# Kernel optimization log

Hardware: AMD Instinct MI355X
Metric: run time of the kernel (lower is better)

## Reference

```python
import jax, jax.numpy as jnp
import numpy as np

NUM_HEADS = 4
HEAD_DIM = 64
RHO = 0.1  # threshold_rho


def setup_inputs() -> dict:
    key = jax.random.key(0)
    k0, k1, k2, k3, k4 = jax.random.split(key, 5)
    B, L, D = 2, 225, 256  # grid_size=15 -> L=225
    Hd = NUM_HEADS * HEAD_DIM
    w_scale = 1.0 / np.sqrt(D)
    return {
        "x": jax.random.normal(k0, (B, L, D), dtype=jnp.float32),
        "Wq": jax.random.normal(k1, (Hd, D), dtype=jnp.float32) * w_scale,
        "Wk": jax.random.normal(k2, (Hd, D), dtype=jnp.float32) * w_scale,
        "Wv": jax.random.normal(k3, (Hd, D), dtype=jnp.float32) * w_scale,
        "Wo": jax.random.normal(k4, (D, Hd), dtype=jnp.float32) * w_scale,
    }


def reference(x, Wq, Wk, Wv, Wo):
    B, L, D = x.shape
    H, d = NUM_HEADS, HEAD_DIM
    # Projections (torch Linear: y = x @ W.T), split heads -> [B,H,L,d]
    q = (x @ Wq.T).reshape(B, L, H, d).transpose(0, 2, 1, 3)
    k = (x @ Wk.T).reshape(B, L, H, d).transpose(0, 2, 1, 3)
    v = (x @ Wv.T).reshape(B, L, H, d).transpose(0, 2, 1, 3)

    # Raw attention scores S = Q K^T  [B,H,L,L]
    S = jnp.einsum('bhid,bhjd->bhij', q, k)

    # Adjacency build: for each key column j, U_j = s_j s_j^T / d, zero diag,
    # keep entries > rho; A = mean over j. Vectorized over j: [B,H,Li,Lk,Lj].
    eye = jnp.eye(L, dtype=S.dtype)
    U = S[:, :, :, None, :] * S[:, :, None, :, :] / d      # [B,H,i,k,j]
    U = U * (1.0 - eye)[None, None, :, :, None]            # zero (i==k) diag
    A = jnp.where(U > RHO, U, 0.0).sum(axis=-1) / L        # [B,H,L,L]

    # Normalize: A_hat = D^-1/2 (A + I) D^-1/2
    A_tilde = A + eye
    deg = jnp.clip(A_tilde.sum(axis=-1, keepdims=True), 1e-6, None)
    d_inv_sqrt = deg ** -0.5
    A_hat = d_inv_sqrt * A_tilde * jnp.swapaxes(d_inv_sqrt, -1, -2)

    # Jump: Phi(S) = A_hat S A_hat^T, then scale and softmax-attend
    S_jump = jnp.einsum('bhij,bhjk,bhlk->bhil', A_hat, S, A_hat) / np.sqrt(d)
    attn = jax.nn.softmax(S_jump, axis=-1)
    out = jnp.einsum('bhij,bhjd->bhid', attn, v)           # [B,H,L,d]
    out = out.transpose(0, 2, 1, 3).reshape(B, L, H * d)
    return out @ Wo.T
```

## Files before the change

### kernel.cpp

```cpp
#include <hip/hip_runtime.h>
#include <math.h>

#define B_  2
#define L_  225
#define D_  256
#define H_  4
#define DH_ 64
#define BH_ (B_*H_)
#define M_  (B_*L_)
#define LL_ (L_*L_)
#define RHO 0.1f
#define INV_L (1.0f/225.0f)
#define INV_SQRT_D 0.125f

__device__ __forceinline__ float dinv_of(const float* deg, int idx) {
    return 1.0f / sqrtf(fmaxf(deg[idx], 1e-6f));
}

__global__ __launch_bounds__(256) void k_qkv(
    const float* __restrict__ x, const float* __restrict__ Wq,
    const float* __restrict__ Wk, const float* __restrict__ Wv,
    float* __restrict__ q, float* __restrict__ k, float* __restrict__ v,
    float* __restrict__ deg)
{
    const int t = threadIdx.x;
    if (blockIdx.z == 0 && blockIdx.y == 0 && t < 128) {
        int idx = blockIdx.x * 128 + t;
        if (idx < BH_ * L_) deg[idx] = 1.0f;
    }
    const int which = blockIdx.z;
    const float* W = (which == 0) ? Wq : (which == 1) ? Wk : Wv;
    float* out = (which == 0) ? q : (which == 1) ? k : v;
    const int m0 = blockIdx.x * 32;
    const int n0 = blockIdx.y * 32;
    __shared__ float Xs[32][36];
    __shared__ float Ws[32][36];
    const int ty = t >> 4, tx = t & 15;
    const int sr = t >> 3, sc4 = (t & 7) * 4;
    float acc[2][2] = {};
    for (int kt = 0; kt < D_; kt += 32) {
        int m = m0 + sr;
        float4 xv = (m < M_) ? *(const float4*)&x[m * D_ + kt + sc4]
                             : make_float4(0.f, 0.f, 0.f, 0.f);
        float4 wv = *(const float4*)&W[(n0 + sr) * D_ + kt + sc4];
        *(float4*)&Xs[sr][sc4] = xv;
        *(float4*)&Ws[sr][sc4] = wv;
        __syncthreads();
        #pragma unroll
        for (int kk = 0; kk < 32; ++kk) {
            float a0 = Xs[ty*2+0][kk], a1 = Xs[ty*2+1][kk];
            float b0 = Ws[tx*2+0][kk], b1 = Ws[tx*2+1][kk];
            acc[0][0] += a0*b0; acc[0][1] += a0*b1;
            acc[1][0] += a1*b0; acc[1][1] += a1*b1;
        }
        __syncthreads();
    }
    #pragma unroll
    for (int i = 0; i < 2; ++i) {
        int m = m0 + ty*2 + i;
        if (m >= M_) continue;
        int b = m / L_, l = m % L_;
        #pragma unroll
        for (int j = 0; j < 2; ++j) {
            int n = n0 + tx*2 + j;
            int h = n >> 6, dd = n & 63;
            out[((b * H_ + h) * L_ + l) * DH_ + dd] = acc[i][j];
        }
    }
}

__global__ __launch_bounds__(256) void k_scores(
    const float* __restrict__ q, const float* __restrict__ kk_,
    float* __restrict__ S)
{
    const int bh = blockIdx.z;
    const int i0 = blockIdx.x * 32, j0 = blockIdx.y * 32;
    __shared__ float Qs[32][68], Ks[32][68];
    const float* qb = q + bh * L_ * DH_;
    const float* kb = kk_ + bh * L_ * DH_;
    const int t = threadIdx.x;
    #pragma unroll
    for (int s = 0; s < 2; ++s) {
        int li = t + s * 256;
        int r = li >> 4, c4 = (li & 15) * 4;
        float4 qv = (i0 + r < L_) ? *(const float4*)&qb[(i0 + r) * DH_ + c4]
                                  : make_float4(0.f,0.f,0.f,0.f);
        float4 kv = (j0 + r < L_) ? *(const float4*)&kb[(j0 + r) * DH_ + c4]
                                  : make_float4(0.f,0.f,0.f,0.f);
        *(float4*)&Qs[r][c4] = qv;
        *(float4*)&Ks[r][c4] = kv;
    }
    __syncthreads();
    const int ty = t >> 4, tx = t & 15;
    float acc[2][2] = {};
    #pragma unroll
    for (int c = 0; c < 64; ++c) {
        float a0 = Qs[ty*2+0][c], a1 = Qs[ty*2+1][c];
        float b0 = Ks[tx*2+0][c], b1 = Ks[tx*2+1][c];
        acc[0][0] += a0*b0; acc[0][1] += a0*b1;
        acc[1][0] += a1*b0; acc[1][1] += a1*b1;
    }
    float* Sb = S + bh * LL_;
    #pragma unroll
    for (int i = 0; i < 2; ++i) {
        int gi = i0 + ty*2 + i;
        if (gi >= L_) continue;
        #pragma unroll
        for (int j = 0; j < 2; ++j) {
            int gj = j0 + tx*2 + j;
            if (gj < L_) Sb[gi * L_ + gj] = acc[i][j];
        }
    }
}

__global__ __launch_bounds__(256) void k_adj(
    const float* __restrict__ S, float* __restrict__ A, float* __restrict__ deg)
{
    const int bh = blockIdx.z;
    const int i0 = blockIdx.x * 32, k0 = blockIdx.y * 32;
    __shared__ float SiT[32][34], SkT[32][34];
    const float* Sb = S + bh * LL_;
    const int t = threadIdx.x;
    const int tx = t & 15, ty = t >> 4;
    float a00 = 0.f, a01 = 0.f, a10 = 0.f, a11 = 0.f;
    for (int jc = 0; jc < L_; jc += 32) {
        #pragma unroll
        for (int s = 0; s < 4; ++s) {
            int li = t + s * 256;
            int r = li >> 5, c = li & 31;
            int j = jc + c;
            SiT[c][r] = (i0 + r < L_ && j < L_) ? Sb[(i0 + r) * L_ + j] * 0.125f : 0.f;
            SkT[c][r] = (k0 + r < L_ && j < L_) ? Sb[(k0 + r) * L_ + j] * 0.125f : 0.f;
        }
        __syncthreads();
        #pragma unroll
        for (int j = 0; j < 32; ++j) {
            float2 a = *(const float2*)&SiT[j][ty * 2];
            float2 b = *(const float2*)&SkT[j][tx * 2];
            float u;
            u = a.x * b.x; a00 += (u > RHO) ? u : 0.f;
            u = a.x * b.y; a01 += (u > RHO) ? u : 0.f;
            u = a.y * b.x; a10 += (u > RHO) ? u : 0.f;
            u = a.y * b.y; a11 += (u > RHO) ? u : 0.f;
        }
        __syncthreads();
    }
    const int gi0 = i0 + ty * 2, gk0 = k0 + tx * 2;
    float v00 = (gi0     < L_ && gk0     < L_ && gi0     != gk0    ) ? a00 * INV_L : 0.f;
    float v01 = (gi0     < L_ && gk0 + 1 < L_ && gi0     != gk0 + 1) ? a01 * INV_L : 0.f;
    float v10 = (gi0 + 1 < L_ && gk0     < L_ && gi0 + 1 != gk0    ) ? a10 * INV_L : 0.f;
    float v11 = (gi0 + 1 < L_ && gk0 + 1 < L_ && gi0 + 1 != gk0 + 1) ? a11 * INV_L : 0.f;
    float* Ab = A + bh * LL_;
    if (gi0 < L_) {
        if (gk0     < L_) Ab[gi0 * L_ + gk0    ] = v00;
        if (gk0 + 1 < L_) Ab[gi0 * L_ + gk0 + 1] = v01;
    }
    if (gi0 + 1 < L_) {
        if (gk0     < L_) Ab[(gi0+1) * L_ + gk0    ] = v10;
        if (gk0 + 1 < L_) Ab[(gi0+1) * L_ + gk0 + 1] = v11;
    }
    float rs0 = v00 + v01, rs1 = v10 + v11;
    #pragma unroll
    for (int m = 1; m < 16; m <<= 1) {
        rs0 += __shfl_xor(rs0, m);
        rs1 += __shfl_xor(rs1, m);
    }
    if (tx == 0) {
        if (gi0     < L_) atomicAdd(&deg[bh * L_ + gi0    ], rs0);
        if (gi0 + 1 < L_) atomicAdd(&deg[bh * L_ + gi0 + 1], rs1);
    }
}

__global__ __launch_bounds__(256) void k_m1(
    const float* __restrict__ A, const float* __restrict__ S,
    const float* __restrict__ deg, float* __restrict__ M1)
{
    const int bh = blockIdx.z;
    const int i0 = blockIdx.x * 32, c0 = blockIdx.y * 32;
    __shared__ float As[32][33];
    __shared__ float Ss[32][34];
    const float* Ab = A + bh * LL_;
    const float* Sb = S + bh * LL_;
    const float* db = deg + bh * L_;
    const int t = threadIdx.x;
    const int ty = t >> 4, tx = t & 15;
    float acc[2][2] = {};
    for (int jt = 0; jt < L_; jt += 32) {
        #pragma unroll
        for (int s = 0; s < 4; ++s) {
            int li = t + s * 256;
            int r = li >> 5, c = li & 31;
            int gi = i0 + r, gj = jt + c;
            float av = (gi < L_ && gj < L_) ? Ab[gi * L_ + gj] : 0.f;
            if (gi == gj && gi < L_) av += 1.f;
            As[r][c] = av;
            int gj2 = jt + r, gc = c0 + c;
            float sv = 0.f;
            if (gj2 < L_ && gc < L_) sv = Sb[gj2 * L_ + gc] * dinv_of(db, gj2);
            Ss[r][c] = sv;
        }
        __syncthreads();
        #pragma unroll
        for (int kk = 0; kk < 32; ++kk) {
            float a0 = As[ty*2+0][kk], a1 = As[ty*2+1][kk];
            float2 b = *(const float2*)&Ss[kk][tx * 2];
            acc[0][0] += a0*b.x; acc[0][1] += a0*b.y;
            acc[1][0] += a1*b.x; acc[1][1] += a1*b.y;
        }
        __syncthreads();
    }
    float* Mb = M1 + bh * LL_;
    #pragma unroll
    for (int i = 0; i < 2; ++i) {
        int gi = i0 + ty*2 + i;
        if (gi >= L_) continue;
        float dvi = dinv_of(db, gi);
        #pragma unroll
        for (int j = 0; j < 2; ++j) {
            int gc = c0 + tx*2 + j;
            if (gc < L_) Mb[gi * L_ + gc] = acc[i][j] * dvi;
        }
    }
}

__global__ __launch_bounds__(256) void k_sjump(
    const float* __restrict__ M1, const float* __restrict__ A,
    const float* __restrict__ deg, float* __restrict__ attn)
{
    const int bh = blockIdx.z;
    const int i0 = blockIdx.x * 32, l0 = blockIdx.y * 32;
    __shared__ float Ms[32][33];
    __shared__ float Bs[32][33];
    const float* Mb = M1 + bh * LL_;
    const float* Ab = A + bh * LL_;
    const float* db = deg + bh * L_;
    const int t = threadIdx.x;
    const int ty = t >> 4, tx = t & 15;
    float acc[2][2] = {};
    for (int jt = 0; jt < L_; jt += 32) {
        #pragma unroll
        for (int s = 0; s < 4; ++s) {
            int li = t + s * 256;
            int r = li >> 5, c = li & 31;
            int gi = i0 + r, gj = jt + c;
            Ms[r][c] = (gi < L_ && gj < L_) ? Mb[gi * L_ + gj] : 0.f;
            int gl = l0 + r;
            float bv = 0.f;
            if (gl < L_ && gj < L_) {
                bv = Ab[gl * L_ + gj];
                if (gl == gj) bv += 1.f;
                bv *= dinv_of(db, gj);
            }
            Bs[r][c] = bv;
        }
        __syncthreads();
        #pragma unroll
        for (int kk = 0; kk < 32; ++kk) {
            float a0 = Ms[ty*2+0][kk], a1 = Ms[ty*2+1][kk];
            float b0 = Bs[tx*2+0][kk], b1 = Bs[tx*2+1][kk];
            acc[0][0] += a0*b0; acc[0][1] += a0*b1;
            acc[1][0] += a1*b0; acc[1][1] += a1*b1;
        }
        __syncthreads();
    }
    float* ob = attn + bh * LL_;
    #pragma unroll
    for (int i = 0; i < 2; ++i) {
        int gi = i0 + ty*2 + i;
        if (gi >= L_) continue;
        #pragma unroll
        for (int j = 0; j < 2; ++j) {
            int gl = l0 + tx*2 + j;
            if (gl < L_) ob[gi * L_ + gl] = acc[i][j] * dinv_of(db, gl) * INV_SQRT_D;
        }
    }
}

__global__ __launch_bounds__(256) void k_smav(
    const float* __restrict__ sj, const float* __restrict__ v,
    float* __restrict__ oh)
{
    const int bh = blockIdx.y, i0 = blockIdx.x * 16;
    __shared__ float P[16][226];
    __shared__ float rinv[16];
    const float* sb = sj + bh * LL_;
    const float* vb = v + bh * L_ * DH_;
    const int t = threadIdx.x;
    for (int e = t; e < 16 * L_; e += 256) {
        int r = e / L_, c = e - r * L_;
        int gi = i0 + r;
        P[r][c] = (gi < L_) ? sb[gi * L_ + c] : 0.f;
    }
    __syncthreads();
    {
        const int r = t >> 4, lane = t & 15;
        float m = -INFINITY;
        for (int c = lane; c < L_; c += 16) m = fmaxf(m, P[r][c]);
        #pragma unroll
        for (int mk = 1; mk < 16; mk <<= 1) m = fmaxf(m, __shfl_xor(m, mk));
        float ssum = 0.f;
        for (int c = lane; c < L_; c += 16) {
            float e = expf(P[r][c] - m);
            P[r][c] = e;
            ssum += e;
        }
        #pragma unroll
        for (int mk = 1; mk < 16; mk <<= 1) ssum += __shfl_xor(ssum, mk);
        if (lane == 0) rinv[r] = 1.0f / ssum;
    }
    __syncthreads();
    const int dd = t & 63, rg = t >> 6;
    float acc[4] = {};
    for (int l = 0; l < L_; ++l) {
        float vv = vb[l * DH_ + dd];
        #pragma unroll
        for (int u = 0; u < 4; ++u) acc[u] += P[rg * 4 + u][l] * vv;
    }
    const int b = bh >> 2, h = bh & 3;
    #pragma unroll
    for (int u = 0; u < 4; ++u) {
        int r = rg * 4 + u;
        int gi = i0 + r;
        if (gi < L_) oh[(b * L_ + gi) * (H_ * DH_) + h * DH_ + dd] = acc[u] * rinv[r];
    }
}

__global__ __launch_bounds__(256) void k_out(
    const float* __restrict__ oh, const float* __restrict__ Wo,
    float* __restrict__ out)
{
    const int m0 = blockIdx.x * 32;
    const int n0 = blockIdx.y * 32;
    __shared__ float Xs[32][36];
    __shared__ float Ws[32][36];
    const int t = threadIdx.x;
    const int ty = t >> 4, tx = t & 15;
    const int sr = t >> 3, sc4 = (t & 7) * 4;
    float acc[2][2] = {};
    for (int kt = 0; kt < D_; kt += 32) {
        int m = m0 + sr;
        float4 xv = (m < M_) ? *(const float4*)&oh[m * D_ + kt + sc4]
                             : make_float4(0.f,0.f,0.f,0.f);
        float4 wv = *(const float4*)&Wo[(n0 + sr) * D_ + kt + sc4];
        *(float4*)&Xs[sr][sc4] = xv;
        *(float4*)&Ws[sr][sc4] = wv;
        __syncthreads();
        #pragma unroll
        for (int kk = 0; kk < 32; ++kk) {
            float a0 = Xs[ty*2+0][kk], a1 = Xs[ty*2+1][kk];
            float b0 = Ws[tx*2+0][kk], b1 = Ws[tx*2+1][kk];
            acc[0][0] += a0*b0; acc[0][1] += a0*b1;
            acc[1][0] += a1*b0; acc[1][1] += a1*b1;
        }
        __syncthreads();
    }
    #pragma unroll
    for (int i = 0; i < 2; ++i) {
        int m = m0 + ty*2 + i;
        if (m >= M_) continue;
        #pragma unroll
        for (int j = 0; j < 2; ++j) {
            int n = n0 + tx*2 + j;
            out[m * D_ + n] = acc[i][j];
        }
    }
}

extern "C" void kernel_launch(void* const* d_in, const int* in_sizes, int n_in,
                              void* d_out, int out_size, void* d_ws, size_t ws_size,
                              hipStream_t stream)
{
    const float* x  = (const float*)d_in[0];
    const float* Wq = (const float*)d_in[1];
    const float* Wk = (const float*)d_in[2];
    const float* Wv = (const float*)d_in[3];
    const float* Wo = (const float*)d_in[4];
    float* out = (float*)d_out;

    float* ws   = (float*)d_ws;
    float* q    = ws;
    float* k    = q    + B_*H_*L_*DH_;
    float* v    = k    + B_*H_*L_*DH_;
    float* S    = v    + B_*H_*L_*DH_;
    float* A    = S    + BH_*LL_;
    float* M1   = A    + BH_*LL_;
    float* attn = M1   + BH_*LL_;
    float* deg  = attn + BH_*LL_;
    float* oh   = deg  + BH_*L_;

    dim3 blk(256);
    k_qkv   <<<dim3(15, 8, 3), blk, 0, stream>>>(x, Wq, Wk, Wv, q, k, v, deg);
    k_scores<<<dim3(8, 8, BH_), blk, 0, stream>>>(q, k, S);
    k_adj   <<<dim3(8, 8, BH_), blk, 0, stream>>>(S, A, deg);
    k_m1    <<<dim3(8, 8, BH_), blk, 0, stream>>>(A, S, deg, M1);
    k_sjump <<<dim3(8, 8, BH_), blk, 0, stream>>>(M1, A, deg, attn);
    k_smav  <<<dim3(15, BH_), blk, 0, stream>>>(attn, v, oh);
    k_out   <<<dim3(15, 8), blk, 0, stream>>>(oh, Wo, out);
}
```

Measured before the change: 199.0 us.

## Fuse all seven stages into one persistent kernel with grid-wide barriers

Replaces the seven separate kernel launches with a single kernel of 512 blocks. Each stage is separated by a software grid barrier built on an atomic counter and spin-waiting, and shared memory is reused across stages through a union. The aim is to remove per-launch overhead and the gaps between small kernels. In exchange it adds a memset, barrier spin latency, and the assumption that all 512 blocks are resident at once; a capped spin prevents a hang but could break correctness if the blocks are not co-resident.

```diff
diff --git a/kernel.cpp b/kernel.cpp
--- a/kernel.cpp
+++ b/kernel.cpp
@@ -13,355 +13,358 @@
 #define INV_L (1.0f/225.0f)
 #define INV_SQRT_D 0.125f
 
+#define NBLK 512
+#define SPIN_MAX 1000000
+
 __device__ __forceinline__ float dinv_of(const float* deg, int idx) {
     return 1.0f / sqrtf(fmaxf(deg[idx], 1e-6f));
 }
 
-__global__ __launch_bounds__(256) void k_qkv(
-    const float* __restrict__ x, const float* __restrict__ Wq,
-    const float* __restrict__ Wk, const float* __restrict__ Wv,
-    float* __restrict__ q, float* __restrict__ k, float* __restrict__ v,
-    float* __restrict__ deg)
+__device__ __forceinline__ void gbar(unsigned* cnt, unsigned target) {
+    __syncthreads();
+    if (threadIdx.x == 0) {
+        __threadfence();
+        __hip_atomic_fetch_add(cnt, 1u, __ATOMIC_ACQ_REL, __HIP_MEMORY_SCOPE_AGENT);
+        int spin = 0;
+        while (__hip_atomic_load(cnt, __ATOMIC_ACQUIRE, __HIP_MEMORY_SCOPE_AGENT) < target) {
+            __builtin_amdgcn_s_sleep(2);
+            if (++spin > SPIN_MAX) break;
+        }
+    }
+    __syncthreads();
+}
+
+struct Args {
+    const float *x, *Wq, *Wk, *Wv, *Wo;
+    float *out, *q, *k, *v, *S, *A, *M1, *attn, *deg, *oh;
+    unsigned *bar;
+};
+
+union alignas(16) Smem {
+    struct { float Xs[32][36]; float Ws[32][36]; } g;
+    struct { float Qs[32][68]; float Ks[32][68]; } sc;
+    struct { float SiT[32][34]; float SkT[32][34]; } adj;
+    struct { float As[32][33]; float Ss[32][34]; } m1;
+    struct { float Ms[32][33]; float Bs[32][33]; } sj;
+    struct { float P[16][226]; float rinv[16]; } sm;
+};
+
+__global__ __launch_bounds__(256, 2) void fused_all(Args a)
 {
+    __shared__ Smem smem;
+    const int b = blockIdx.x;
     const int t = threadIdx.x;
-    if (blockIdx.z == 0 && blockIdx.y == 0 && t < 128) {
-        int idx = blockIdx.x * 128 + t;
-        if (idx < BH_ * L_) deg[idx] = 1.0f;
-    }
-    const int which = blockIdx.z;
-    const float* W = (which == 0) ? Wq : (which == 1) ? Wk : Wv;
-    float* out = (which == 0) ? q : (which == 1) ? k : v;
-    const int m0 = blockIdx.x * 32;
-    const int n0 = blockIdx.y * 32;
-    __shared__ float Xs[32][36];
-    __shared__ float Ws[32][36];
-    const int ty = t >> 4, tx = t & 15;
-    const int sr = t >> 3, sc4 = (t & 7) * 4;
-    float acc[2][2] = {};
-    for (int kt = 0; kt < D_; kt += 32) {
-        int m = m0 + sr;
-        float4 xv = (m < M_) ? *(const float4*)&x[m * D_ + kt + sc4]
-                             : make_float4(0.f, 0.f, 0.f, 0.f);
-        float4 wv = *(const float4*)&W[(n0 + sr) * D_ + kt + sc4];
-        *(float4*)&Xs[sr][sc4] = xv;
-        *(float4*)&Ws[sr][sc4] = wv;
+
+    if (b < 360) {
+        const int which = b / 120;
+        const int r = b - which * 120;
+        const int m0 = (r % 15) * 32, n0 = (r / 15) * 32;
+        const float* W = (which == 0) ? a.Wq : (which == 1) ? a.Wk : a.Wv;
+        float* out = (which == 0) ? a.q : (which == 1) ? a.k : a.v;
+        const int ty = t >> 4, tx = t & 15;
+        const int sr = t >> 3, sc4 = (t & 7) * 4;
+        float acc[2][2] = {};
+        for (int kt = 0; kt < D_; kt += 32) {
+            int m = m0 + sr;
+            float4 xv = (m < M_) ? *(const float4*)&a.x[m * D_ + kt + sc4]
+                                 : make_float4(0.f, 0.f, 0.f, 0.f);
+            float4 wv = *(const float4*)&W[(n0 + sr) * D_ + kt + sc4];
+            *(float4*)&smem.g.Xs[sr][sc4] = xv;
+            *(float4*)&smem.g.Ws[sr][sc4] = wv;
+            __syncthreads();
+            #pragma unroll
+            for (int kk = 0; kk < 32; ++kk) {
+                float a0 = smem.g.Xs[ty*2+0][kk], a1 = smem.g.Xs[ty*2+1][kk];
+                float b0 = smem.g.Ws[tx*2+0][kk], b1 = smem.g.Ws[tx*2+1][kk];
+                acc[0][0] += a0*b0; acc[0][1] += a0*b1;
+                acc[1][0] += a1*b0; acc[1][1] += a1*b1;
+            }
+            __syncthreads();
+        }
+        #pragma unroll
+        for (int i = 0; i < 2; ++i) {
+            int m = m0 + ty*2 + i;
+            if (m >= M_) continue;
+            int bb = m / L_, l = m % L_;
+            #pragma unroll
+            for (int j = 0; j < 2; ++j) {
+                int n = n0 + tx*2 + j;
+                int h = n >> 6, dd = n & 63;
+                out[((bb * H_ + h) * L_ + l) * DH_ + dd] = acc[i][j];
+            }
+        }
+    } else if (b < 368) {
+        int idx = (b - 360) * 256 + t;
+        if (idx < BH_ * L_) a.deg[idx] = 1.0f;
+    }
+    gbar(a.bar, NBLK * 1);
+
+    {
+        const int bh = b >> 6, rr = b & 63;
+        const int i0 = (rr >> 3) * 32, j0 = (rr & 7) * 32;
+        const float* qb = a.q + bh * L_ * DH_;
+        const float* kb = a.k + bh * L_ * DH_;
+        #pragma unroll
+        for (int s = 0; s < 2; ++s) {
+            int li = t + s * 256;
+            int r = li >> 4, c4 = (li & 15) * 4;
+            float4 qv = (i0 + r < L_) ? *(const float4*)&qb[(i0 + r) * DH_ + c4]
+                                      : make_float4(0.f,0.f,0.f,0.f);
+            float4 kv = (j0 + r < L_) ? *(const float4*)&kb[(j0 + r) * DH_ + c4]
+                                      : make_float4(0.f,0.f,0.f,0.f);
+            *(float4*)&smem.sc.Qs[r][c4] = qv;
+            *(float4*)&smem.sc.Ks[r][c4] = kv;
+        }
         __syncthreads();
-        #pragma unroll
-        for (int kk = 0; kk < 32; ++kk) {
-            float a0 = Xs[ty*2+0][kk], a1 = Xs[ty*2+1][kk];
-            float b0 = Ws[tx*2+0][kk], b1 = Ws[tx*2+1][kk];
+        const int ty = t >> 4, tx = t & 15;
+        float acc[2][2] = {};
+        #pragma unroll
+        for (int c = 0; c < 64; ++c) {
+            float a0 = smem.sc.Qs[ty*2+0][c], a1 = smem.sc.Qs[ty*2+1][c];
+            float b0 = smem.sc.Ks[tx*2+0][c], b1 = smem.sc.Ks[tx*2+1][c];
             acc[0][0] += a0*b0; acc[0][1] += a0*b1;
             acc[1][0] += a1*b0; acc[1][1] += a1*b1;
         }
+        float* Sb = a.S + bh * LL_;
+        #pragma unroll
+        for (int i = 0; i < 2; ++i) {
+            int gi = i0 + ty*2 + i;
+            if (gi >= L_) continue;
+            #pragma unroll
+            for (int j = 0; j < 2; ++j) {
+                int gj = j0 + tx*2 + j;
+                if (gj < L_) Sb[gi * L_ + gj] = acc[i][j];
+            }
+        }
+    }
+    gbar(a.bar, NBLK * 2);
+
+    {
+        const int bh = b >> 6, rr = b & 63;
+        const int i0 = (rr >> 3) * 32, k0 = (rr & 7) * 32;
+        const float* Sb = a.S + bh * LL_;
+        const int tx = t & 15, ty = t >> 4;
+        float a00 = 0.f, a01 = 0.f, a10 = 0.f, a11 = 0.f;
+        for (int jc = 0; jc < L_; jc += 32) {
+            #pragma unroll
+            for (int s = 0; s < 4; ++s) {
+                int li = t + s * 256;
+                int r = li >> 5, c = li & 31;
+                int j = jc + c;
+                smem.adj.SiT[c][r] = (i0 + r < L_ && j < L_) ? Sb[(i0 + r) * L_ + j] * 0.125f : 0.f;
+                smem.adj.SkT[c][r] = (k0 + r < L_ && j < L_) ? Sb[(k0 + r) * L_ + j] * 0.125f : 0.f;
+            }
+            __syncthreads();
+            #pragma unroll
+            for (int j = 0; j < 32; ++j) {
+                float2 av = *(const float2*)&smem.adj.SiT[j][ty * 2];
+                float2 bv = *(const float2*)&smem.adj.SkT[j][tx * 2];
+                float u;
+                u = av.x * bv.x; a00 += (u > RHO) ? u : 0.f;
+                u = av.x * bv.y; a01 += (u > RHO) ? u : 0.f;
+                u = av.y * bv.x; a10 += (u > RHO) ? u : 0.f;
+                u = av.y * bv.y; a11 += (u > RHO) ? u : 0.f;
+            }
+            __syncthreads();
+        }
+        const int gi0 = i0 + ty * 2, gk0 = k0 + tx * 2;
+        float v00 = (gi0     < L_ && gk0     < L_ && gi0     != gk0    ) ? a00 * INV_L : 0.f;
+        float v01 = (gi0     < L_ && gk0 + 1 < L_ && gi0     != gk0 + 1) ? a01 * INV_L : 0.f;
+        float v10 = (gi0 + 1 < L_ && gk0     < L_ && gi0 + 1 != gk0    ) ? a10 * INV_L : 0.f;
+        float v11 = (gi0 + 1 < L_ && gk0 + 1 < L_ && gi0 + 1 != gk0 + 1) ? a11 * INV_L : 0.f;
+        float* Ab = a.A + bh * LL_;
+        if (gi0 < L_) {
+            if (gk0     < L_) Ab[gi0 * L_ + gk0    ] = v00;
+            if (gk0 + 1 < L_) Ab[gi0 * L_ + gk0 + 1] = v01;
+        }
+        if (gi0 + 1 < L_) {
+            if (gk0     < L_) Ab[(gi0+1) * L_ + gk0    ] = v10;
+            if (gk0 + 1 < L_) Ab[(gi0+1) * L_ + gk0 + 1] = v11;
+        }
+        float rs0 = v00 + v01, rs1 = v10 + v11;
+        #pragma unroll
+        for (int m = 1; m < 16; m <<= 1) {
+            rs0 += __shfl_xor(rs0, m);
+            rs1 += __shfl_xor(rs1, m);
+        }
+        if (tx == 0) {
+            if (gi0     < L_) atomicAdd(&a.deg[bh * L_ + gi0    ], rs0);
+            if (gi0 + 1 < L_) atomicAdd(&a.deg[bh * L_ + gi0 + 1], rs1);
+        }
+    }
+    gbar(a.bar, NBLK * 3);
+
+    {
+        const int bh = b >> 6, rr = b & 63;
+        const int i0 = (rr >> 3) * 32, c0 = (rr & 7) * 32;
+        const float* Ab = a.A + bh * LL_;
+        const float* Sb = a.S + bh * LL_;
+        const float* db = a.deg + bh * L_;
+        const int ty = t >> 4, tx = t & 15;
+        float acc[2][2] = {};
+        for (int jt = 0; jt < L_; jt += 32) {
+            #pragma unroll
+            for (int s = 0; s < 4; ++s) {
+                int li = t + s * 256;
+                int r = li >> 5, c = li & 31;
+                int gi = i0 + r, gj = jt + c;
+                float av = (gi < L_ && gj < L_) ? Ab[gi * L_ + gj] : 0.f;
+                if (gi == gj && gi < L_) av += 1.f;
+                smem.m1.As[r][c] = av;
+                int gj2 = jt + r, gc = c0 + c;
+                float sv = 0.f;
+                if (gj2 < L_ && gc < L_) sv = Sb[gj2 * L_ + gc] * dinv_of(db, gj2);
+                smem.m1.Ss[r][c] = sv;
+            }
+            __syncthreads();
+            #pragma unroll
+            for (int kk = 0; kk < 32; ++kk) {
+                float a0 = smem.m1.As[ty*2+0][kk], a1 = smem.m1.As[ty*2+1][kk];
+                float2 bv = *(const float2*)&smem.m1.Ss[kk][tx * 2];
+                acc[0][0] += a0*bv.x; acc[0][1] += a0*bv.y;
+                acc[1][0] += a1*bv.x; acc[1][1] += a1*bv.y;
+            }
+            __syncthreads();
+        }
+        float* Mb = a.M1 + bh * LL_;
+        #pragma unroll
+        for (int i = 0; i < 2; ++i) {
+            int gi = i0 + ty*2 + i;
+            if (gi >= L_) continue;
+            float dvi = dinv_of(db, gi);
+            #pragma unroll
+            for (int j = 0; j < 2; ++j) {
+                int gc = c0 + tx*2 + j;
+                if (gc < L_) Mb[gi * L_ + gc] = acc[i][j] * dvi;
+            }
+        }
+    }
+    gbar(a.bar, NBLK * 4);
+
+    {
+        const int bh = b >> 6, rr = b & 63;
+        const int i0 = (rr >> 3) * 32, l0 = (rr & 7) * 32;
+        const float* Mb = a.M1 + bh * LL_;
+        const float* Ab = a.A + bh * LL_;
+        const float* db = a.deg + bh * L_;
+        const int ty = t >> 4, tx = t & 15;
+        float acc[2][2] = {};
+        for (int jt = 0; jt < L_; jt += 32) {
+            #pragma unroll
+            for (int s = 0; s < 4; ++s) {
+                int li = t + s * 256;
+                int r = li >> 5, c = li & 31;
+                int gi = i0 + r, gj = jt + c;
+                smem.sj.Ms[r][c] = (gi < L_ && gj < L_) ? Mb[gi * L_ + gj] : 0.f;
+                int gl = l0 + r;
+                float bv = 0.f;
+                if (gl < L_ && gj < L_) {
+                    bv = Ab[gl * L_ + gj];
+                    if (gl == gj) bv += 1.f;
+                    bv *= dinv_of(db, gj);
+                }
+                smem.sj.Bs[r][c] = bv;
+            }
+            __syncthreads();
+            #pragma unroll
+            for (int kk = 0; kk < 32; ++kk) {
+                float a0 = smem.sj.Ms[ty*2+0][kk], a1 = smem.sj.Ms[ty*2+1][kk];
+                float b0 = smem.sj.Bs[tx*2+0][kk], b1 = smem.sj.Bs[tx*2+1][kk];
+                acc[0][0] += a0*b0; acc[0][1] += a0*b1;
+                acc[1][0] += a1*b0; acc[1][1] += a1*b1;
+            }
+            __syncthreads();
+        }
+        float* ob = a.attn + bh * LL_;
+        #pragma unroll
+        for (int i = 0; i < 2; ++i) {
+            int gi = i0 + ty*2 + i;
+            if (gi >= L_) continue;
+            #pragma unroll
+            for (int j = 0; j < 2; ++j) {
+                int gl = l0 + tx*2 + j;
+                if (gl < L_) ob[gi * L_ + gl] = acc[i][j] * dinv_of(db, gl) * INV_SQRT_D;
+            }
+        }
+    }
+    gbar(a.bar, NBLK * 5);
+
+    if (b < 120) {
+        const int bh = b / 15, i0 = (b % 15) * 16;
+        const float* sb = a.attn + bh * LL_;
+        const float* vb = a.v + bh * L_ * DH_;
+        for (int e = t; e < 16 * L_; e += 256) {
+            int r = e / L_, c = e - r * L_;
+            int gi = i0 + r;
+            smem.sm.P[r][c] = (gi < L_) ? sb[gi * L_ + c] : 0.f;
+        }
         __syncthreads();
-    }
-    #pragma unroll
-    for (int i = 0; i < 2; ++i) {
-        int m = m0 + ty*2 + i;
-        if (m >= M_) continue;
-        int b = m / L_, l = m % L_;
-        #pragma unroll
-        for (int j = 0; j < 2; ++j) {
-            int n = n0 + tx*2 + j;
-            int h = n >> 6, dd = n & 63;
-            out[((b * H_ + h) * L_ + l) * DH_ + dd] = acc[i][j];
-        }
-    }
-}
-
-__global__ __launch_bounds__(256) void k_scores(
-    const float* __restrict__ q, const float* __restrict__ kk_,
-    float* __restrict__ S)
-{
-    const int bh = blockIdx.z;
-    const int i0 = blockIdx.x * 32, j0 = blockIdx.y * 32;
-    __shared__ float Qs[32][68], Ks[32][68];
-    const float* qb = q + bh * L_ * DH_;
-    const float* kb = kk_ + bh * L_ * DH_;
-    const int t = threadIdx.x;
-    #pragma unroll
-    for (int s = 0; s < 2; ++s) {
-        int li = t + s * 256;
-        int r = li >> 4, c4 = (li & 15) * 4;
-        float4 qv = (i0 + r < L_) ? *(const float4*)&qb[(i0 + r) * DH_ + c4]
-                                  : make_float4(0.f,0.f,0.f,0.f);
-        float4 kv = (j0 + r < L_) ? *(const float4*)&kb[(j0 + r) * DH_ + c4]
-                                  : make_float4(0.f,0.f,0.f,0.f);
-        *(float4*)&Qs[r][c4] = qv;
-        *(float4*)&Ks[r][c4] = kv;
-    }
-    __syncthreads();
-    const int ty = t >> 4, tx = t & 15;
-    float acc[2][2] = {};
-    #pragma unroll
-    for (int c = 0; c < 64; ++c) {
-        float a0 = Qs[ty*2+0][c], a1 = Qs[ty*2+1][c];
-        float b0 = Ks[tx*2+0][c], b1 = Ks[tx*2+1][c];
-        acc[0][0] += a0*b0; acc[0][1] += a0*b1;
-        acc[1][0] += a1*b0; acc[1][1] += a1*b1;
-    }
-    float* Sb = S + bh * LL_;
-    #pragma unroll
-    for (int i = 0; i < 2; ++i) {
-        int gi = i0 + ty*2 + i;
-        if (gi >= L_) continue;
-        #pragma unroll
-        for (int j = 0; j < 2; ++j) {
-            int gj = j0 + tx*2 + j;
-            if (gj < L_) Sb[gi * L_ + gj] = acc[i][j];
-        }
-    }
-}
-
-__global__ __launch_bounds__(256) void k_adj(
-    const float* __restrict__ S, float* __restrict__ A, float* __restrict__ deg)
-{
-    const int bh = blockIdx.z;
-    const int i0 = blockIdx.x * 32, k0 = blockIdx.y * 32;
-    __shared__ float SiT[32][34], SkT[32][34];
-    const float* Sb = S + bh * LL_;
-    const int t = threadIdx.x;
-    const int tx = t & 15, ty = t >> 4;
-    float a00 = 0.f, a01 = 0.f, a10 = 0.f, a11 = 0.f;
-    for (int jc = 0; jc < L_; jc += 32) {
-        #pragma unroll
-        for (int s = 0; s < 4; ++s) {
-            int li = t + s * 256;
-            int r = li >> 5, c = li & 31;
-            int j = jc + c;
-            SiT[c][r] = (i0 + r < L_ && j < L_) ? Sb[(i0 + r) * L_ + j] * 0.125f : 0.f;
-            SkT[c][r] = (k0 + r < L_ && j < L_) ? Sb[(k0 + r) * L_ + j] * 0.125f : 0.f;
+        {
+            const int r = t >> 4, lane = t & 15;
+            float m = -INFINITY;
+            for (int c = lane; c < L_; c += 16) m = fmaxf(m, smem.sm.P[r][c]);
+            #pragma unroll
+            for (int mk = 1; mk < 16; mk <<= 1) m = fmaxf(m, __shfl_xor(m, mk));
+            float ssum = 0.f;
+            for (int c = lane; c < L_; c += 16) {
+                float e = expf(smem.sm.P[r][c] - m);
+                smem.sm.P[r][c] = e;
+                ssum += e;
+            }
+            #pragma unroll
+            for (int mk = 1; mk < 16; mk <<= 1) ssum += __shfl_xor(ssum, mk);
+            if (lane == 0) smem.sm.rinv[r] = 1.0f / ssum;
         }
         __syncthreads();
-        #pragma unroll
-        for (int j = 0; j < 32; ++j) {
-            float2 a = *(const float2*)&SiT[j][ty * 2];
-            float2 b = *(const float2*)&SkT[j][tx * 2];
-            float u;
-            u = a.x * b.x; a00 += (u > RHO) ? u : 0.f;
-            u = a.x * b.y; a01 += (u > RHO) ? u : 0.f;
-            u = a.y * b.x; a10 += (u > RHO) ? u : 0.f;
-            u = a.y * b.y; a11 += (u > RHO) ? u : 0.f;
-        }
-        __syncthreads();
-    }
-    const int gi0 = i0 + ty * 2, gk0 = k0 + tx * 2;
-    float v00 = (gi0     < L_ && gk0     < L_ && gi0     != gk0    ) ? a00 * INV_L : 0.f;
-    float v01 = (gi0     < L_ && gk0 + 1 < L_ && gi0     != gk0 + 1) ? a01 * INV_L : 0.f;
-    float v10 = (gi0 + 1 < L_ && gk0     < L_ && gi0 + 1 != gk0    ) ? a10 * INV_L : 0.f;
-    float v11 = (gi0 + 1 < L_ && gk0 + 1 < L_ && gi0 + 1 != gk0 + 1) ? a11 * INV_L : 0.f;
-    float* Ab = A + bh * LL_;
-    if (gi0 < L_) {
-        if (gk0     < L_) Ab[gi0 * L_ + gk0    ] = v00;
-        if (gk0 + 1 < L_) Ab[gi0 * L_ + gk0 + 1] = v01;
-    }
-    if (gi0 + 1 < L_) {
-        if (gk0     < L_) Ab[(gi0+1) * L_ + gk0    ] = v10;
-        if (gk0 + 1 < L_) Ab[(gi0+1) * L_ + gk0 + 1] = v11;
-    }
-    float rs0 = v00 + v01, rs1 = v10 + v11;
-    #pragma unroll
-    for (int m = 1; m < 16; m <<= 1) {
-        rs0 += __shfl_xor(rs0, m);
-        rs1 += __shfl_xor(rs1, m);
-    }
-    if (tx == 0) {
-        if (gi0     < L_) atomicAdd(&deg[bh * L_ + gi0    ], rs0);
-        if (gi0 + 1 < L_) atomicAdd(&deg[bh * L_ + gi0 + 1], rs1);
-    }
-}
-
-__global__ __launch_bounds__(256) void k_m1(
-    const float* __restrict__ A, const float* __restrict__ S,
-    const float* __restrict__ deg, float* __restrict__ M1)
-{
-    const int bh = blockIdx.z;
-    const int i0 = blockIdx.x * 32, c0 = blockIdx.y * 32;
-    __shared__ float As[32][33];
-    __shared__ float Ss[32][34];
-    const float* Ab = A + bh * LL_;
-    const float* Sb = S + bh * LL_;
-    const float* db = deg + bh * L_;
-    const int t = threadIdx.x;
-    const int ty = t >> 4, tx = t & 15;
-    float acc[2][2] = {};
-    for (int jt = 0; jt < L_; jt += 32) {
-        #pragma unroll
-        for (int s = 0; s < 4; ++s) {
-            int li = t + s * 256;
-            int r = li >> 5, c = li & 31;
-            int gi = i0 + r, gj = jt + c;
-            float av = (gi < L_ && gj < L_) ? Ab[gi * L_ + gj] : 0.f;
-            if (gi == gj && gi < L_) av += 1.f;
-            As[r][c] = av;
-            int gj2 = jt + r, gc = c0 + c;
-            float sv = 0.f;
-            if (gj2 < L_ && gc < L_) sv = Sb[gj2 * L_ + gc] * dinv_of(db, gj2);
-            Ss[r][c] = sv;
-        }
-        __syncthreads();
-        #pragma unroll
-        for (int kk = 0; kk < 32; ++kk) {
-            float a0 = As[ty*2+0][kk], a1 = As[ty*2+1][kk];
-            float2 b = *(const float2*)&Ss[kk][tx * 2];
-            acc[0][0] += a0*b.x; acc[0][1] += a0*b.y;
-            acc[1][0] += a1*b.x; acc[1][1] += a1*b.y;
-        }
-        __syncthreads();
-    }
-    float* Mb = M1 + bh * LL_;
-    #pragma unroll
-    for (int i = 0; i < 2; ++i) {
-        int gi = i0 + ty*2 + i;
-        if (gi >= L_) continue;
-        float dvi = dinv_of(db, gi);
-        #pragma unroll
-        for (int j = 0; j < 2; ++j) {
-            int gc = c0 + tx*2 + j;
-            if (gc < L_) Mb[gi * L_ + gc] = acc[i][j] * dvi;
-        }
-    }
-}
-
-__global__ __launch_bounds__(256) void k_sjump(
-    const float* __restrict__ M1, const float* __restrict__ A,
-    const float* __restrict__ deg, float* __restrict__ attn)
-{
-    const int bh = blockIdx.z;
-    const int i0 = blockIdx.x * 32, l0 = blockIdx.y * 32;
-    __shared__ float Ms[32][33];
-    __shared__ float Bs[32][33];
-    const float* Mb = M1 + bh * LL_;
-    const float* Ab = A + bh * LL_;
-    const float* db = deg + bh * L_;
-    const int t = threadIdx.x;
-    const int ty = t >> 4, tx = t & 15;
-    float acc[2][2] = {};
-    for (int jt = 0; jt < L_; jt += 32) {
-        #pragma unroll
-        for (int s = 0; s < 4; ++s) {
-            int li = t + s * 256;
-            int r = li >> 5, c = li & 31;
-            int gi = i0 + r, gj = jt + c;
-            Ms[r][c] = (gi < L_ && gj < L_) ? Mb[gi * L_ + gj] : 0.f;
-            int gl = l0 + r;
-            float bv = 0.f;
-            if (gl < L_ && gj < L_) {
-                bv = Ab[gl * L_ + gj];
-                if (gl == gj) bv += 1.f;
-                bv *= dinv_of(db, gj);
-            }
-            Bs[r][c] = bv;
-        }
-        __syncthreads();
-        #pragma unroll
-        for (int kk = 0; kk < 32; ++kk) {
-            float a0 = Ms[ty*2+0][kk], a1 = Ms[ty*2+1][kk];
-            float b0 = Bs[tx*2+0][kk], b1 = Bs[tx*2+1][kk];
-            acc[0][0] += a0*b0; acc[0][1] += a0*b1;
-            acc[1][0] += a1*b0; acc[1][1] += a1*b1;
-        }
-        __syncthreads();
-    }
-    float* ob = attn + bh * LL_;
-    #pragma unroll
-    for (int i = 0; i < 2; ++i) {
-        int gi = i0 + ty*2 + i;
-        if (gi >= L_) continue;
-        #pragma unroll
-        for (int j = 0; j < 2; ++j) {
-            int gl = l0 + tx*2 + j;
-            if (gl < L_) ob[gi * L_ + gl] = acc[i][j] * dinv_of(db, gl) * INV_SQRT_D;
-        }
-    }
-}
-
-__global__ __launch_bounds__(256) void k_smav(
-    const float* __restrict__ sj, const float* __restrict__ v,
-    float* __restrict__ oh)
-{
-    const int bh = blockIdx.y, i0 = blockIdx.x * 16;
-    __shared__ float P[16][226];
-    __shared__ float rinv[16];
-    const float* sb = sj + bh * LL_;
-    const float* vb = v + bh * L_ * DH_;
-    const int t = threadIdx.x;
-    for (int e = t; e < 16 * L_; e += 256) {
-        int r = e / L_, c = e - r * L_;
-        int gi = i0 + r;
-        P[r][c] = (gi < L_) ? sb[gi * L_ + c] : 0.f;
-    }
-    __syncthreads();
-    {
-        const int r = t >> 4, lane = t & 15;
-        float m = -INFINITY;
-        for (int c = lane; c < L_; c += 16) m = fmaxf(m, P[r][c]);
-        #pragma unroll
-        for (int mk = 1; mk < 16; mk <<= 1) m = fmaxf(m, __shfl_xor(m, mk));
-        float ssum = 0.f;
-        for (int c = lane; c < L_; c += 16) {
-            float e = expf(P[r][c] - m);
-            P[r][c] = e;
-            ssum += e;
-        }
-        #pragma unroll
-        for (int mk = 1; mk < 16; mk <<= 1) ssum += __shfl_xor(ssum, mk);
-        if (lane == 0) rinv[r] = 1.0f / ssum;
-    }
-    __syncthreads();
-    const int dd = t & 63, rg = t >> 6;
-    float acc[4] = {};
-    for (int l = 0; l < L_; ++l) {
-        float vv = vb[l * DH_ + dd];
-        #pragma unroll
-        for (int u = 0; u < 4; ++u) acc[u] += P[rg * 4 + u][l] * vv;
-    }
-    const int b = bh >> 2, h = bh & 3;
-    #pragma unroll
-    for (int u = 0; u < 4; ++u) {
-        int r = rg * 4 + u;
-        int gi = i0 + r;
-        if (gi < L_) oh[(b * L_ + gi) * (H_ * DH_) + h * DH_ + dd] = acc[u] * rinv[r];
-    }
-}
-
-__global__ __launch_bounds__(256) void k_out(
-    const float* __restrict__ oh, const float* __restrict__ Wo,
-    float* __restrict__ out)
-{
-    const int m0 = blockIdx.x * 32;
-    const int n0 = blockIdx.y * 32;
-    __shared__ float Xs[32][36];
-    __shared__ float Ws[32][36];
-    const int t = threadIdx.x;
-    const int ty = t >> 4, tx = t & 15;
-    const int sr = t >> 3, sc4 = (t & 7) * 4;
-    float acc[2][2] = {};
-    for (int kt = 0; kt < D_; kt += 32) {
-        int m = m0 + sr;
-        float4 xv = (m < M_) ? *(const float4*)&oh[m * D_ + kt + sc4]
-                             : make_float4(0.f,0.f,0.f,0.f);
-        float4 wv = *(const float4*)&Wo[(n0 + sr) * D_ + kt + sc4];
-        *(float4*)&Xs[sr][sc4] = xv;
-        *(float4*)&Ws[sr][sc4] = wv;
-        __syncthreads();
-        #pragma unroll
-        for (int kk = 0; kk < 32; ++kk) {
-            float a0 = Xs[ty*2+0][kk], a1 = Xs[ty*2+1][kk];
-            float b0 = Ws[tx*2+0][kk], b1 = Ws[tx*2+1][kk];
-            acc[0][0] += a0*b0; acc[0][1] += a0*b1;
-            acc[1][0] += a1*b0; acc[1][1] += a1*b1;
-        }
-        __syncthreads();
-    }
-    #pragma unroll
-    for (int i = 0; i < 2; ++i) {
-        int m = m0 + ty*2 + i;
-        if (m >= M_) continue;
-        #pragma unroll
-        for (int j = 0; j < 2; ++j) {
-            int n = n0 + tx*2 + j;
-            out[m * D_ + n] = acc[i][j];
+        const int dd = t & 63, rg = t >> 6;
+        float acc[4] = {};
+        for (int l = 0; l < L_; ++l) {
+            float vv = vb[l * DH_ + dd];
+            #pragma unroll
+            for (int u = 0; u < 4; ++u) acc[u] += smem.sm.P[rg * 4 + u][l] * vv;
+        }
+        const int bb = bh >> 2, h = bh & 3;
+        #pragma unroll
+        for (int u = 0; u < 4; ++u) {
+            int r = rg * 4 + u;
+            int gi = i0 + r;
+            if (gi < L_) a.oh[(bb * L_ + gi) * (H_ * DH_) + h * DH_ + dd]
+                             = acc[u] * smem.sm.rinv[r];
+        }
+    }
+    gbar(a.bar, NBLK * 6);
+
+    if (b < 120) {
+        const int m0 = (b % 15) * 32, n0 = (b / 15) * 32;
+        const int ty = t >> 4, tx = t & 15;
+        const int sr = t >> 3, sc4 = (t & 7) * 4;
+        float acc[2][2] = {};
+        for (int kt = 0; kt < D_; kt += 32) {
+            int m = m0 + sr;
+            float4 xv = (m < M_) ? *(const float4*)&a.oh[m * D_ + kt + sc4]
+                                 : make_float4(0.f,0.f,0.f,0.f);
+            float4 wv = *(const float4*)&a.Wo[(n0 + sr) * D_ + kt + sc4];
+            *(float4*)&smem.g.Xs[sr][sc4] = xv;
+            *(float4*)&smem.g.Ws[sr][sc4] = wv;
+            __syncthreads();
+            #pragma unroll
+            for (int kk = 0; kk < 32; ++kk) {
+                float a0 = smem.g.Xs[ty*2+0][kk], a1 = smem.g.Xs[ty*2+1][kk];
+                float b0 = smem.g.Ws[tx*2+0][kk], b1 = smem.g.Ws[tx*2+1][kk];
+                acc[0][0] += a0*b0; acc[0][1] += a0*b1;
+                acc[1][0] += a1*b0; acc[1][1] += a1*b1;
+            }
+            __syncthreads();
+        }
+        #pragma unroll
+        for (int i = 0; i < 2; ++i) {
+            int m = m0 + ty*2 + i;
+            if (m >= M_) continue;
+            #pragma unroll
+            for (int j = 0; j < 2; ++j) {
+                int n = n0 + tx*2 + j;
+                a.out[m * D_ + n] = acc[i][j];
+            }
         }
     }
 }
@@ -387,13 +390,14 @@
     float* attn = M1   + BH_*LL_;
     float* deg  = attn + BH_*LL_;
     float* oh   = deg  + BH_*L_;
-
-    dim3 blk(256);
-    k_qkv   <<<dim3(15, 8, 3), blk, 0, stream>>>(x, Wq, Wk, Wv, q, k, v, deg);
-    k_scores<<<dim3(8, 8, BH_), blk, 0, stream>>>(q, k, S);
-    k_adj   <<<dim3(8, 8, BH_), blk, 0, stream>>>(S, A, deg);
-    k_m1    <<<dim3(8, 8, BH_), blk, 0, stream>>>(A, S, deg, M1);
-    k_sjump <<<dim3(8, 8, BH_), blk, 0, stream>>>(M1, A, deg, attn);
-    k_smav  <<<dim3(15, BH_), blk, 0, stream>>>(attn, v, oh);
-    k_out   <<<dim3(15, 8), blk, 0, stream>>>(oh, Wo, out);
+    unsigned* bar = (unsigned*)(oh + M_*D_);
+
+    hipMemsetAsync(bar, 0, 256, stream);
+
+    Args ha;
+    ha.x = x; ha.Wq = Wq; ha.Wk = Wk; ha.Wv = Wv; ha.Wo = Wo;
+    ha.out = out; ha.q = q; ha.k = k; ha.v = v; ha.S = S; ha.A = A;
+    ha.M1 = M1; ha.attn = attn; ha.deg = deg; ha.oh = oh; ha.bar = bar;
+
+    fused_all<<<dim3(NBLK), dim3(256), 0, stream>>>(ha);
 }
```

Measured after the change: 594.8 us. +198.9%, slower.
